# Kernel tuning notes

Measured on AMD Instinct MI355X. Metric: run time of the kernel, lower is better.

## Reference

```python
import jax, jax.numpy as jnp
import numpy as np

IN, H, C, B = 1024, 1024, 16, 4096


def setup_inputs() -> dict:
    key = jax.random.key(0)
    ks = jax.random.split(key, 5)
    s = 1.0 / np.sqrt(IN)
    sh = 1.0 / np.sqrt(H)
    return {
        "input_word": jax.random.normal(ks[0], (B, IN), dtype=jnp.float32),
        "hidden_states": jax.random.normal(ks[1], (B, H), dtype=jnp.float32),
        # stacked per-cell Linear weights (torch Linear: y = x @ W.T + b)
        "Wx": jax.random.uniform(ks[2], (C, 2 * H, IN), jnp.float32, -s, s),
        "bx": jax.random.uniform(ks[3], (C, 2 * H), jnp.float32, -s, s),
        "Wh": jax.random.uniform(ks[4], (C, 2 * H, H), jnp.float32, -sh, sh),
    }


def reference(input_word, hidden_states, Wx, bx, Wh):
    # all cells active (entity_mask all ones, domain_tag='Source')
    # net[b,c,o] = sum_i x[b,i] Wx[c,o,i] + bx[c,o] + sum_h h[b,h] Wh[c,o,h]
    net = (jnp.einsum('bi,coi->bco', input_word, Wx)
           + jnp.einsum('bh,coh->bco', hidden_states, Wh)
           + bx[None, :, :])  # [B, C, 2H]
    input_gate, cell_states = net[..., :H], net[..., H:]
    cell_input = jnp.tanh(cell_states)
    input_gate = jax.nn.sigmoid(input_gate)
    return (cell_input, input_gate)
```

## Files before the change

### kernel.cpp

```cpp
#include <hip/hip_runtime.h>
#include <hip/hip_bf16.h>

#define IN_DIM 1024
#define H_DIM  1024
#define C_DIM  16
#define B_DIM  4096
#define K_DIM  2048
#define N_DIM  32768
#define M_DIM  4096
#define NT     32

typedef __attribute__((ext_vector_type(8))) short short8;
typedef __attribute__((ext_vector_type(4))) float f32x4;

__device__ __forceinline__ unsigned short f2bf_rne(float f) {
  union { float f; unsigned u; } a; a.f = f;
  unsigned r = a.u + 0x7FFFu + ((a.u >> 16) & 1u);
  return (unsigned short)(r >> 16);
}

__global__ void convert_pack_kernel(const float* __restrict__ xs,
                                    const float* __restrict__ hs,
                                    unsigned short* __restrict__ out,
                                    int rows) {
  long total = (long)rows * (K_DIM / 8);
  for (long i = blockIdx.x * (long)blockDim.x + threadIdx.x; i < total;
       i += (long)gridDim.x * blockDim.x) {
    long e = i * 8;
    int r = (int)(e >> 11);
    int k = (int)(e & 2047);
    const float* src = (k < IN_DIM) ? (xs + (long)r * IN_DIM + k)
                                    : (hs + (long)r * H_DIM + (k - IN_DIM));
    float4 v0 = *(const float4*)(src);
    float4 v1 = *(const float4*)(src + 4);
    union { unsigned short u[8]; short8 s; } p;
    p.u[0] = f2bf_rne(v0.x); p.u[1] = f2bf_rne(v0.y);
    p.u[2] = f2bf_rne(v0.z); p.u[3] = f2bf_rne(v0.w);
    p.u[4] = f2bf_rne(v1.x); p.u[5] = f2bf_rne(v1.y);
    p.u[6] = f2bf_rne(v1.z); p.u[7] = f2bf_rne(v1.w);
    *(short8*)(out + e) = p.s;
  }
}

__device__ __forceinline__ void dma16(const short* g, int ldsOff) {
  asm volatile("s_mov_b32 m0, %1\n\t"
               "global_load_lds_dwordx4 %0, off"
               :: "v"(g), "s"(ldsOff) : "memory");
}

__global__ void __launch_bounds__(512, 2)
gemm_act_kernel(const short* __restrict__ A,
                const short* __restrict__ Bt,
                const float* __restrict__ bias,
                float* __restrict__ out) {
  extern __shared__ short lds[];

  int cpx = (int)gridDim.x >> 3;
  int wg  = ((int)blockIdx.x & 7) * cpx + ((int)blockIdx.x >> 3);
  int mt = wg & 15;
  int nt = wg >> 4;
  int m0 = mt * 256;
  int n0 = nt * 256;

  const int tid  = (int)threadIdx.x;
  const int lane = tid & 63;
  const int wid  = tid >> 6;
  const int wr   = wid >> 2;
  const int wc   = wid & 3;

  const int crow = (lane >> 4) * 4;
  const int ccol = lane & 15;
  const long HALF = (long)B_DIM * C_DIM * H_DIM;
  float bia[4]; int cg[4], og[4];
#pragma unroll
  for (int ni = 0; ni < 4; ++ni) {
    int gn = n0 + wc * 64 + ni * 16 + ccol;
    bia[ni] = bias[gn];
    cg[ni] = gn >> 11;
    og[ni] = gn & 2047;
  }

  const int srow = tid >> 3;
  const int sc   = (tid & 7) ^ (srow & 7);
  const short* Abase = A  + (long)(m0 + srow) * K_DIM + sc * 8;
  const short* Bbase = Bt + (long)(n0 + srow) * K_DIM + sc * 8;
  const int wb = __builtin_amdgcn_readfirstlane((tid >> 6) * 1024);

  auto stA = [&](int kt, int r0, int buf) {
    dma16(Abase + (long)r0 * K_DIM + kt * 64, buf * 32768 + r0 * 128 + wb);
  };
  auto stB = [&](int kt, int r0, int buf) {
    dma16(Bbase + (long)r0 * K_DIM + kt * 64, 65536 + buf * 32768 + r0 * 128 + wb);
  };

  const int fr = lane & 15;
  const int g8 = lane >> 4;
  int aoffS[8][2], boffS[4][2];
#pragma unroll
  for (int mi = 0; mi < 8; ++mi) {
    int r = wr * 128 + mi * 16 + fr;
#pragma unroll
    for (int kk = 0; kk < 2; ++kk)
      aoffS[mi][kk] = r * 64 + (((kk * 4 + g8) ^ (r & 7)) << 3);
  }
#pragma unroll
  for (int ni = 0; ni < 4; ++ni) {
    int r = wc * 64 + ni * 16 + fr;
#pragma unroll
    for (int kk = 0; kk < 2; ++kk)
      boffS[ni][kk] = r * 64 + (((kk * 4 + g8) ^ (r & 7)) << 3);
  }

  f32x4 acc[8][4] = {};

  stA(0, 0, 0); stA(0, 64, 0); stA(0, 128, 0); stA(0, 192, 0);
  stB(0, 0, 0); stB(0, 64, 0); stB(0, 128, 0); stB(0, 192, 0);
  stB(1, 0, 1); stB(1, 64, 1); stB(1, 128, 1); stB(1, 192, 1);
  stA(1, 0, 1); stA(1, 128, 1);
  asm volatile("s_waitcnt vmcnt(6)" ::: "memory");
  __builtin_amdgcn_s_barrier();

  auto iter = [&](int t, int cur) {
    const bool s1 = (t + 1) < NT;
    const bool s2 = (t + 2) < NT;
    const short* cA = lds + cur * 16384;
    const short* cB = lds + 32768 + cur * 16384;
    const int nx = cur ^ 1;
    short8 av[4], bv0[4], bv1[4];
#pragma unroll
    for (int i = 0; i < 4; ++i) av[i]  = *(const short8*)(cA + aoffS[i][0]);
#pragma unroll
    for (int j = 0; j < 4; ++j) bv0[j] = *(const short8*)(cB + boffS[j][0]);
    if (s1) stA(t + 1, 64, nx);
    __builtin_amdgcn_s_setprio(1);
#pragma unroll
    for (int i = 0; i < 4; ++i)
#pragma unroll
      for (int j = 0; j < 4; ++j)
        acc[i][j] = __builtin_amdgcn_mfma_f32_16x16x32_bf16(av[i], bv0[j], acc[i][j], 0, 0, 0);
    __builtin_amdgcn_s_setprio(0);
    __builtin_amdgcn_s_barrier();
#pragma unroll
    for (int i = 0; i < 4; ++i) av[i]  = *(const short8*)(cA + aoffS[i][1]);
#pragma unroll
    for (int j = 0; j < 4; ++j) bv1[j] = *(const short8*)(cB + boffS[j][1]);
    if (s1) stA(t + 1, 192, nx);
    __builtin_amdgcn_s_setprio(1);
#pragma unroll
    for (int i = 0; i < 4; ++i)
#pragma unroll
      for (int j = 0; j < 4; ++j)
        acc[i][j] = __builtin_amdgcn_mfma_f32_16x16x32_bf16(av[i], bv1[j], acc[i][j], 0, 0, 0);
    __builtin_amdgcn_s_setprio(0);
    __builtin_amdgcn_s_barrier();
#pragma unroll
    for (int i = 0; i < 4; ++i) av[i] = *(const short8*)(cA + aoffS[4 + i][0]);
    if (s2) { stB(t + 2, 0, cur); stB(t + 2, 64, cur); stA(t + 2, 0, cur); }
    __builtin_amdgcn_s_setprio(1);
#pragma unroll
    for (int i = 0; i < 4; ++i)
#pragma unroll
      for (int j = 0; j < 4; ++j)
        acc[4 + i][j] = __builtin_amdgcn_mfma_f32_16x16x32_bf16(av[i], bv0[j], acc[4 + i][j], 0, 0, 0);
    __builtin_amdgcn_s_setprio(0);
    __builtin_amdgcn_s_barrier();
#pragma unroll
    for (int i = 0; i < 4; ++i) av[i] = *(const short8*)(cA + aoffS[4 + i][1]);
    if (s2) { stB(t + 2, 128, cur); stB(t + 2, 192, cur); stA(t + 2, 128, cur); }
    __builtin_amdgcn_s_setprio(1);
#pragma unroll
    for (int i = 0; i < 4; ++i)
#pragma unroll
      for (int j = 0; j < 4; ++j)
        acc[4 + i][j] = __builtin_amdgcn_mfma_f32_16x16x32_bf16(av[i], bv1[j], acc[4 + i][j], 0, 0, 0);
    __builtin_amdgcn_s_setprio(0);
    if (s2)      asm volatile("s_waitcnt vmcnt(6)" ::: "memory");
    else if (s1) asm volatile("s_waitcnt vmcnt(0)" ::: "memory");
    __builtin_amdgcn_s_barrier();
  };

  for (int t = 0; t < NT; t += 2) {
    iter(t,     0);
    iter(t + 1, 1);
  }

#pragma unroll
  for (int mi = 0; mi < 8; ++mi) {
    int gb0 = m0 + wr * 128 + mi * 16 + crow;
#pragma unroll
    for (int ni = 0; ni < 4; ++ni) {
      int c = cg[ni], o = og[ni];
#pragma unroll
      for (int j = 0; j < 4; ++j) {
        float v = acc[mi][ni][j] + bia[ni];
        long b = gb0 + j;
        if (o < H_DIM) {
          float r = 1.0f / (1.0f + __expf(-v));
          __builtin_nontemporal_store(r, &out[HALF + (b * C_DIM + c) * H_DIM + o]);
        } else {
          float av2 = fabsf(v);
          float e = __expf(-2.0f * av2);
          float r = (1.0f - e) / (1.0f + e);
          r = (v < 0.0f) ? -r : r;
          __builtin_nontemporal_store(r, &out[(b * C_DIM + c) * H_DIM + (o - H_DIM)]);
        }
      }
    }
  }
}

__global__ void fallback_kernel(const float* __restrict__ x,
                                const float* __restrict__ h,
                                const float* __restrict__ Wx,
                                const float* __restrict__ bx,
                                const float* __restrict__ Wh,
                                float* __restrict__ out) {
  int b = blockIdx.x;
  int c = blockIdx.y;
  __shared__ float lx[IN_DIM], lh[H_DIM];
  for (int i = threadIdx.x; i < IN_DIM; i += blockDim.x) {
    lx[i] = x[(long)b * IN_DIM + i];
    lh[i] = h[(long)b * H_DIM + i];
  }
  __syncthreads();
  const long HALF = (long)B_DIM * C_DIM * H_DIM;
  for (int o = threadIdx.x; o < 2 * H_DIM; o += blockDim.x) {
    const float* wx = Wx + ((long)c * 2 * H_DIM + o) * IN_DIM;
    const float* wh = Wh + ((long)c * 2 * H_DIM + o) * H_DIM;
    float acc = bx[c * 2 * H_DIM + o];
    for (int k = 0; k < IN_DIM; ++k) acc += lx[k] * wx[k];
    for (int k = 0; k < H_DIM; ++k) acc += lh[k] * wh[k];
    if (o < H_DIM) {
      out[HALF + ((long)b * C_DIM + c) * H_DIM + o] = 1.0f / (1.0f + __expf(-acc));
    } else {
      float av = fabsf(acc);
      float t = __expf(-2.0f * av);
      float r = (1.0f - t) / (1.0f + t);
      out[((long)b * C_DIM + c) * H_DIM + (o - H_DIM)] = (acc < 0.0f) ? -r : r;
    }
  }
}

extern "C" void kernel_launch(void* const* d_in, const int* in_sizes, int n_in,
                              void* d_out, int out_size, void* d_ws, size_t ws_size,
                              hipStream_t stream) {
  const float* x  = (const float*)d_in[0];
  const float* h  = (const float*)d_in[1];
  const float* Wx = (const float*)d_in[2];
  const float* bx = (const float*)d_in[3];
  const float* Wh = (const float*)d_in[4];
  float* out = (float*)d_out;

  const size_t needA = (size_t)M_DIM * K_DIM * sizeof(short);
  const size_t needB = (size_t)N_DIM * K_DIM * sizeof(short);
  if (ws_size < needA + needB) {
    dim3 g(B_DIM, C_DIM);
    fallback_kernel<<<g, 256, 0, stream>>>(x, h, Wx, bx, Wh, out);
    return;
  }

  unsigned short* Abf = (unsigned short*)d_ws;
  unsigned short* Bbf = (unsigned short*)((char*)d_ws + needA);

  convert_pack_kernel<<<2048, 256, 0, stream>>>(x, h, Abf, M_DIM);
  convert_pack_kernel<<<4096, 256, 0, stream>>>(Wx, Wh, Bbf, N_DIM);

  (void)hipFuncSetAttribute((const void*)gemm_act_kernel,
                            hipFuncAttributeMaxDynamicSharedMemorySize, 131072);
  gemm_act_kernel<<<2048, 512, 131072, stream>>>((const short*)Abf, (const short*)Bbf,
                                                 bx, out);
}
```

Before: 735.1 us.

## Double-buffer LDS fragments in registers to overlap loads with MFMA phases

Restructures the GEMM main loop so the LDS-to-register fragment loads for the next MFMA phase are issued before the current phase's MFMAs. It uses two A register sets and preloads the first fragments of the next k-tile at the end of each iteration. Global-to-LDS prefetches are now unconditional with a clamped tile index, so the tail branches disappear. The waitcnt points are moved, and per-row offset arrays are replaced by one base offset plus a constant stride, which saves registers. The cost is more live vector registers, redundant DMA traffic in the last iterations, and tighter reliance on the hand-tuned vmcnt values being correct.

Result: faster. 709.9 us (-3.4%).

```diff
diff --git a/kernel.cpp b/kernel.cpp
--- a/kernel.cpp
+++ b/kernel.cpp
@@ -95,23 +95,29 @@
 
   const int fr = lane & 15;
   const int g8 = lane >> 4;
-  int aoffS[8][2], boffS[4][2];
-#pragma unroll
-  for (int mi = 0; mi < 8; ++mi) {
-    int r = wr * 128 + mi * 16 + fr;
-#pragma unroll
-    for (int kk = 0; kk < 2; ++kk)
-      aoffS[mi][kk] = r * 64 + (((kk * 4 + g8) ^ (r & 7)) << 3);
-  }
-#pragma unroll
-  for (int ni = 0; ni < 4; ++ni) {
-    int r = wc * 64 + ni * 16 + fr;
-#pragma unroll
-    for (int kk = 0; kk < 2; ++kk)
-      boffS[ni][kk] = r * 64 + (((kk * 4 + g8) ^ (r & 7)) << 3);
-  }
+  int aoff0[2], boff0[2];
+#pragma unroll
+  for (int kk = 0; kk < 2; ++kk) {
+    aoff0[kk] = (wr * 128 + fr) * 64 + (((kk * 4 + g8) ^ (fr & 7)) << 3);
+    boff0[kk] = (wc * 64  + fr) * 64 + (((kk * 4 + g8) ^ (fr & 7)) << 3);
+  }
+  auto lda = [&](int buf, int mi, int kk) {
+    return *(const short8*)(lds + buf * 16384 + aoff0[kk] + mi * 1024);
+  };
+  auto ldb = [&](int buf, int ni, int kk) {
+    return *(const short8*)(lds + 32768 + buf * 16384 + boff0[kk] + ni * 1024);
+  };
 
   f32x4 acc[8][4] = {};
+  short8 avA[4], avB[4], bv0[4], bv1[4];
+
+  auto mfma4 = [&](short8 (&a)[4], short8 (&b)[4], int mb) {
+#pragma unroll
+    for (int i = 0; i < 4; ++i)
+#pragma unroll
+      for (int j = 0; j < 4; ++j)
+        acc[mb + i][j] = __builtin_amdgcn_mfma_f32_16x16x32_bf16(a[i], b[j], acc[mb + i][j], 0, 0, 0);
+  };
 
   stA(0, 0, 0); stA(0, 64, 0); stA(0, 128, 0); stA(0, 192, 0);
   stB(0, 0, 0); stB(0, 64, 0); stB(0, 128, 0); stB(0, 192, 0);
@@ -119,70 +125,55 @@
   stA(1, 0, 1); stA(1, 128, 1);
   asm volatile("s_waitcnt vmcnt(6)" ::: "memory");
   __builtin_amdgcn_s_barrier();
-
-  auto iter = [&](int t, int cur) {
-    const bool s1 = (t + 1) < NT;
-    const bool s2 = (t + 2) < NT;
-    const short* cA = lds + cur * 16384;
-    const short* cB = lds + 32768 + cur * 16384;
-    const int nx = cur ^ 1;
-    short8 av[4], bv0[4], bv1[4];
-#pragma unroll
-    for (int i = 0; i < 4; ++i) av[i]  = *(const short8*)(cA + aoffS[i][0]);
-#pragma unroll
-    for (int j = 0; j < 4; ++j) bv0[j] = *(const short8*)(cB + boffS[j][0]);
-    if (s1) stA(t + 1, 64, nx);
-    __builtin_amdgcn_s_setprio(1);
-#pragma unroll
-    for (int i = 0; i < 4; ++i)
-#pragma unroll
-      for (int j = 0; j < 4; ++j)
-        acc[i][j] = __builtin_amdgcn_mfma_f32_16x16x32_bf16(av[i], bv0[j], acc[i][j], 0, 0, 0);
-    __builtin_amdgcn_s_setprio(0);
-    __builtin_amdgcn_s_barrier();
-#pragma unroll
-    for (int i = 0; i < 4; ++i) av[i]  = *(const short8*)(cA + aoffS[i][1]);
-#pragma unroll
-    for (int j = 0; j < 4; ++j) bv1[j] = *(const short8*)(cB + boffS[j][1]);
-    if (s1) stA(t + 1, 192, nx);
-    __builtin_amdgcn_s_setprio(1);
-#pragma unroll
-    for (int i = 0; i < 4; ++i)
-#pragma unroll
-      for (int j = 0; j < 4; ++j)
-        acc[i][j] = __builtin_amdgcn_mfma_f32_16x16x32_bf16(av[i], bv1[j], acc[i][j], 0, 0, 0);
-    __builtin_amdgcn_s_setprio(0);
-    __builtin_amdgcn_s_barrier();
-#pragma unroll
-    for (int i = 0; i < 4; ++i) av[i] = *(const short8*)(cA + aoffS[4 + i][0]);
-    if (s2) { stB(t + 2, 0, cur); stB(t + 2, 64, cur); stA(t + 2, 0, cur); }
-    __builtin_amdgcn_s_setprio(1);
-#pragma unroll
-    for (int i = 0; i < 4; ++i)
-#pragma unroll
-      for (int j = 0; j < 4; ++j)
-        acc[4 + i][j] = __builtin_amdgcn_mfma_f32_16x16x32_bf16(av[i], bv0[j], acc[4 + i][j], 0, 0, 0);
-    __builtin_amdgcn_s_setprio(0);
-    __builtin_amdgcn_s_barrier();
-#pragma unroll
-    for (int i = 0; i < 4; ++i) av[i] = *(const short8*)(cA + aoffS[4 + i][1]);
-    if (s2) { stB(t + 2, 128, cur); stB(t + 2, 192, cur); stA(t + 2, 128, cur); }
-    __builtin_amdgcn_s_setprio(1);
-#pragma unroll
-    for (int i = 0; i < 4; ++i)
-#pragma unroll
-      for (int j = 0; j < 4; ++j)
-        acc[4 + i][j] = __builtin_amdgcn_mfma_f32_16x16x32_bf16(av[i], bv1[j], acc[4 + i][j], 0, 0, 0);
-    __builtin_amdgcn_s_setprio(0);
-    if (s2)      asm volatile("s_waitcnt vmcnt(6)" ::: "memory");
-    else if (s1) asm volatile("s_waitcnt vmcnt(0)" ::: "memory");
+#pragma unroll
+  for (int i = 0; i < 4; ++i) avA[i] = lda(0, i, 0);
+#pragma unroll
+  for (int j = 0; j < 4; ++j) bv0[j] = ldb(0, j, 0);
+
+  auto iter = [&](int t, int cur, int nx) {
+    const int t1 = (t + 1 < NT) ? t + 1 : NT - 1;
+    const int t2 = (t + 2 < NT) ? t + 2 : NT - 1;
+#pragma unroll
+    for (int i = 0; i < 4; ++i) avB[i] = lda(cur, i, 1);
+#pragma unroll
+    for (int j = 0; j < 4; ++j) bv1[j] = ldb(cur, j, 1);
+    stA(t1, 64, nx);
+    __builtin_amdgcn_s_setprio(1);
+    mfma4(avA, bv0, 0);
+    __builtin_amdgcn_s_setprio(0);
+    asm volatile("s_waitcnt vmcnt(7)" ::: "memory");
+    __builtin_amdgcn_s_barrier();
+#pragma unroll
+    for (int i = 0; i < 4; ++i) avA[i] = lda(cur, 4 + i, 0);
+    stA(t1, 192, nx);
+    __builtin_amdgcn_s_setprio(1);
+    mfma4(avB, bv1, 0);
+    __builtin_amdgcn_s_setprio(0);
+    __builtin_amdgcn_s_barrier();
+#pragma unroll
+    for (int i = 0; i < 4; ++i) avB[i] = lda(cur, 4 + i, 1);
+    stB(t2, 0, cur); stB(t2, 64, cur); stA(t2, 0, cur);
+    __builtin_amdgcn_s_setprio(1);
+    mfma4(avA, bv0, 4);
+    __builtin_amdgcn_s_setprio(0);
+    asm volatile("s_waitcnt vmcnt(5)" ::: "memory");
+    __builtin_amdgcn_s_barrier();
+#pragma unroll
+    for (int i = 0; i < 4; ++i) avA[i] = lda(nx, i, 0);
+#pragma unroll
+    for (int j = 0; j < 4; ++j) bv0[j] = ldb(nx, j, 0);
+    stB(t2, 128, cur); stB(t2, 192, cur); stA(t2, 128, cur);
+    __builtin_amdgcn_s_setprio(1);
+    mfma4(avB, bv1, 4);
+    __builtin_amdgcn_s_setprio(0);
     __builtin_amdgcn_s_barrier();
   };
 
   for (int t = 0; t < NT; t += 2) {
-    iter(t,     0);
-    iter(t + 1, 1);
-  }
+    iter(t,     0, 1);
+    iter(t + 1, 1, 0);
+  }
+  asm volatile("s_waitcnt vmcnt(0)" ::: "memory");
 
 #pragma unroll
   for (int mi = 0; mi < 8; ++mi) {
```
